# Kernel tuning notes

Hardware: AMD Instinct MI355X
Metric: run time of the kernel (lower is better)

The kernel has to match this reference:

```python
import jax, jax.numpy as jnp
import numpy as np

H = W = 2048
C = 8
N = 1_000_000


def setup_inputs() -> dict:
    key = jax.random.key(0)
    k1, k2 = jax.random.split(key)
    # coords in [0, H-4); the forward's mod wraps any value into range anyway
    coords = jax.random.uniform(k1, (N, 2), dtype=jnp.float32) * (H - 4)
    visible = jax.random.normal(k2, (H, W, C), dtype=jnp.float32)
    return {"coords": coords, "visible": visible}


def reference(coords, visible):
    dims = jnp.asarray(visible.shape[:2], dtype=coords.dtype)  # [2] = (H, W)
    # wrap coordinates into [1, dim-3) exactly like the TF layer
    c = ((coords - 1.0) % (dims - 4.0)) + 1.0          # [N,2]
    idx_low = jnp.floor(c)
    delta = c - idx_low                                 # [N,2]
    i = idx_low.astype(jnp.int32)                       # [N,2]

    def g(di, dj):  # gather visible at idx_low + [di, dj] -> [N,C]
        return visible[i[:, 0] + di, i[:, 1] + dj]

    top_left, top_right = g(0, 0), g(1, 0)
    bottom_left, bottom_right = g(0, 1), g(1, 1)

    d0 = delta[:, :1]   # delta along first coord axis, [N,1]
    d1 = delta[:, 1:2]  # delta along second coord axis, [N,1]

    mid_bottom = bottom_right + d0 * (bottom_left - bottom_right)
    mid_top = top_right + d0 * (top_left - top_right)
    interpolation = mid_bottom + d1 * (mid_top - mid_bottom)  # [N,C]

    # boundary mask exactly as in source (compares only coord 0; mod makes it a no-op)
    off = c > dims                                       # [N,2]
    cond = jnp.logical_or(off[:, 0], off[:, 0])          # [N]
    return jnp.where(cond[:, None], jnp.zeros_like(interpolation), interpolation)
```

## Files before the change

kernel.cpp:

```cpp
#include <hip/hip_runtime.h>

#define HH 2048
#define WW 2048
#define CC 8
#define MODV 2044.0f

__device__ __forceinline__ float lerp3(float tl, float tr, float bl, float br,
                                       float d0, float d1) {
    float mb = br + d0 * (bl - br);
    float mt = tr + d0 * (tl - tr);
    return mb + d1 * (mt - mb);
}

__global__ __launch_bounds__(256) void idx2pixel_kernel(
    const float* __restrict__ coords,
    const float* __restrict__ visible,
    float* __restrict__ out,
    int n)
{
    int t = blockIdx.x * blockDim.x + threadIdx.x;
    if (t >= n) return;

    float2 co = *reinterpret_cast<const float2*>(coords + 2 * (size_t)t);

    float x = co.x - 1.0f;
    float y = co.y - 1.0f;
    float cx = fmodf(x, MODV); if (cx < 0.0f) cx += MODV;
    float cy = fmodf(y, MODV); if (cy < 0.0f) cy += MODV;
    cx += 1.0f;
    cy += 1.0f;

    float fx = floorf(cx);
    float fy = floorf(cy);
    float d0 = cx - fx;
    float d1 = cy - fy;
    int i0 = (int)fx;
    int i1 = (int)fy;

    const float* p00 = visible + ((size_t)i0 * WW + (size_t)i1) * CC;
    const float* p01 = p00 + CC;
    const float* p10 = p00 + (size_t)WW * CC;
    const float* p11 = p10 + CC;

    float4 tl0 = *reinterpret_cast<const float4*>(p00);
    float4 tl1 = *reinterpret_cast<const float4*>(p00 + 4);
    float4 bl0 = *reinterpret_cast<const float4*>(p01);
    float4 bl1 = *reinterpret_cast<const float4*>(p01 + 4);
    float4 tr0 = *reinterpret_cast<const float4*>(p10);
    float4 tr1 = *reinterpret_cast<const float4*>(p10 + 4);
    float4 br0 = *reinterpret_cast<const float4*>(p11);
    float4 br1 = *reinterpret_cast<const float4*>(p11 + 4);

    bool zero = cx > (float)HH;
    float m = zero ? 0.0f : 1.0f;

    float4 o0, o1;
    o0.x = m * lerp3(tl0.x, tr0.x, bl0.x, br0.x, d0, d1);
    o0.y = m * lerp3(tl0.y, tr0.y, bl0.y, br0.y, d0, d1);
    o0.z = m * lerp3(tl0.z, tr0.z, bl0.z, br0.z, d0, d1);
    o0.w = m * lerp3(tl0.w, tr0.w, bl0.w, br0.w, d0, d1);
    o1.x = m * lerp3(tl1.x, tr1.x, bl1.x, br1.x, d0, d1);
    o1.y = m * lerp3(tl1.y, tr1.y, bl1.y, br1.y, d0, d1);
    o1.z = m * lerp3(tl1.z, tr1.z, bl1.z, br1.z, d0, d1);
    o1.w = m * lerp3(tl1.w, tr1.w, bl1.w, br1.w, d0, d1);

    float* po = out + (size_t)t * CC;
    *reinterpret_cast<float4*>(po)     = o0;
    *reinterpret_cast<float4*>(po + 4) = o1;
}

extern "C" void kernel_launch(void* const* d_in, const int* in_sizes, int n_in,
                              void* d_out, int out_size, void* d_ws, size_t ws_size,
                              hipStream_t stream) {
    const float* coords  = (const float*)d_in[0];
    const float* visible = (const float*)d_in[1];
    float* out = (float*)d_out;
    int n = in_sizes[0] / 2;

    int block = 256;
    int grid = (n + block - 1) / block;
    idx2pixel_kernel<<<grid, block, 0, stream>>>(coords, visible, out, n);
}
```

Baseline: 227.8 us.

## Split each point's bilinear gather across four cooperating lanes with shuffle combine

Assigns four threads per output point. Each lane loads one 16-byte quarter of the two adjacent-row pixel pairs, giving a contiguous 32-byte segment per row. Each lane lerps along d0, then combines with its neighbour via __shfl_xor, and two lanes write the output. This is meant to raise memory-level parallelism and coalescing for the random gathers, at the cost of four times as many threads, redundant coordinate math in each lane, and idle lanes during the store.

```diff
diff --git a/kernel.cpp b/kernel.cpp
--- a/kernel.cpp
+++ b/kernel.cpp
@@ -5,68 +5,48 @@
 #define CC 8
 #define MODV 2044.0f
 
-__device__ __forceinline__ float lerp3(float tl, float tr, float bl, float br,
-                                       float d0, float d1) {
-    float mb = br + d0 * (bl - br);
-    float mt = tr + d0 * (tl - tr);
-    return mb + d1 * (mt - mb);
-}
+typedef float f32x2 __attribute__((ext_vector_type(2)));
+typedef float f32x4 __attribute__((ext_vector_type(4)));
 
-__global__ __launch_bounds__(256) void idx2pixel_kernel(
+__global__ __launch_bounds__(256) void idx2pixel_coop(
     const float* __restrict__ coords,
     const float* __restrict__ visible,
     float* __restrict__ out,
     int n)
 {
-    int t = blockIdx.x * blockDim.x + threadIdx.x;
-    if (t >= n) return;
+    int tid = blockIdx.x * 256 + threadIdx.x;
+    int point = tid >> 2;
+    int c = threadIdx.x & 3;
+    if (point >= n) return;
 
-    float2 co = *reinterpret_cast<const float2*>(coords + 2 * (size_t)t);
+    f32x2 co = reinterpret_cast<const f32x2*>(coords)[point];
 
-    float x = co.x - 1.0f;
-    float y = co.y - 1.0f;
-    float cx = fmodf(x, MODV); if (cx < 0.0f) cx += MODV;
-    float cy = fmodf(y, MODV); if (cy < 0.0f) cy += MODV;
-    cx += 1.0f;
-    cy += 1.0f;
-
+    float cx = fmodf(co.x - 1.0f, MODV); if (cx < 0.0f) cx += MODV; cx += 1.0f;
+    float cy = fmodf(co.y - 1.0f, MODV); if (cy < 0.0f) cy += MODV; cy += 1.0f;
     float fx = floorf(cx);
     float fy = floorf(cy);
     float d0 = cx - fx;
     float d1 = cy - fy;
     int i0 = (int)fx;
     int i1 = (int)fy;
+    float m = (cx > (float)HH) ? 0.0f : 1.0f;
 
-    const float* p00 = visible + ((size_t)i0 * WW + (size_t)i1) * CC;
-    const float* p01 = p00 + CC;
-    const float* p10 = p00 + (size_t)WW * CC;
-    const float* p11 = p10 + CC;
+    const float* p = visible + ((size_t)i0 * WW + (size_t)i1) * CC + c * 4;
+    f32x4 rA = *(const f32x4*)(p);
+    f32x4 rB = *(const f32x4*)(p + (size_t)WW * CC);
 
-    float4 tl0 = *reinterpret_cast<const float4*>(p00);
-    float4 tl1 = *reinterpret_cast<const float4*>(p00 + 4);
-    float4 bl0 = *reinterpret_cast<const float4*>(p01);
-    float4 bl1 = *reinterpret_cast<const float4*>(p01 + 4);
-    float4 tr0 = *reinterpret_cast<const float4*>(p10);
-    float4 tr1 = *reinterpret_cast<const float4*>(p10 + 4);
-    float4 br0 = *reinterpret_cast<const float4*>(p11);
-    float4 br1 = *reinterpret_cast<const float4*>(p11 + 4);
+    f32x4 v = rB + d0 * (rA - rB);
 
-    bool zero = cx > (float)HH;
-    float m = zero ? 0.0f : 1.0f;
+    f32x4 w;
+    w.x = __shfl_xor(v.x, 2, 64);
+    w.y = __shfl_xor(v.y, 2, 64);
+    w.z = __shfl_xor(v.z, 2, 64);
+    w.w = __shfl_xor(v.w, 2, 64);
 
-    float4 o0, o1;
-    o0.x = m * lerp3(tl0.x, tr0.x, bl0.x, br0.x, d0, d1);
-    o0.y = m * lerp3(tl0.y, tr0.y, bl0.y, br0.y, d0, d1);
-    o0.z = m * lerp3(tl0.z, tr0.z, bl0.z, br0.z, d0, d1);
-    o0.w = m * lerp3(tl0.w, tr0.w, bl0.w, br0.w, d0, d1);
-    o1.x = m * lerp3(tl1.x, tr1.x, bl1.x, br1.x, d0, d1);
-    o1.y = m * lerp3(tl1.y, tr1.y, bl1.y, br1.y, d0, d1);
-    o1.z = m * lerp3(tl1.z, tr1.z, bl1.z, br1.z, d0, d1);
-    o1.w = m * lerp3(tl1.w, tr1.w, bl1.w, br1.w, d0, d1);
-
-    float* po = out + (size_t)t * CC;
-    *reinterpret_cast<float4*>(po)     = o0;
-    *reinterpret_cast<float4*>(po + 4) = o1;
+    if (c < 2) {
+        f32x4 o = m * (w + d1 * (v - w));
+        *(f32x4*)(out + (size_t)point * CC + c * 4) = o;
+    }
 }
 
 extern "C" void kernel_launch(void* const* d_in, const int* in_sizes, int n_in,
@@ -77,7 +57,6 @@
     float* out = (float*)d_out;
     int n = in_sizes[0] / 2;
 
-    int block = 256;
-    int grid = (n + block - 1) / block;
-    idx2pixel_kernel<<<grid, block, 0, stream>>>(coords, visible, out, n);
+    int grid = (n + 63) / 64;
+    idx2pixel_coop<<<grid, 256, 0, stream>>>(coords, visible, out, n);
 }
```

Result: faster. 215.7 us (median of 2 runs) (-5.3%).
